# Performance work log

Hardware: AMD Instinct MI355X
Metric: run time of the kernel (lower is better)

Reference implementation:

```python
import jax, jax.numpy as jnp
import numpy as np

N = 10000   # nodes
E = 160000  # edges
F_IN = 768  # input features
EPS = 1e-5


def _norm_weights(src, dst, ew, n):
    # sym-normalized scaled Laplacian with lambda_max=2: T_hat = -D^{-1/2} A D^{-1/2}
    deg = jax.ops.segment_sum(ew, src, num_segments=n)
    deg_safe = jnp.where(deg > 0, deg, 1.0)
    dis = jnp.where(deg > 0, jax.lax.rsqrt(deg_safe), 0.0)
    return -dis[src] * ew * dis[dst]


def _cheb(x, src, dst, norm, Ws, b, n):
    # PyG ChebConv forward: out = sum_k lin_k(T_k(L_hat) x) + bias
    def prop(h):  # gather -> weight -> scatter-add
        return jax.ops.segment_sum(norm[:, None] * h[src], dst, num_segments=n)
    Tx0 = x
    out = Tx0 @ Ws[0]
    if len(Ws) > 1:
        Tx1 = prop(Tx0)
        out = out + Tx1 @ Ws[1]
        for W in Ws[2:]:
            Tx2 = 2.0 * prop(Tx1) - Tx0
            out = out + Tx2 @ W
            Tx0, Tx1 = Tx1, Tx2
    return out + b


def _bn(x, g, b):
    # training-mode batch norm over the node dim
    mu = x.mean(axis=0)
    var = x.var(axis=0)
    return (x - mu) * jax.lax.rsqrt(var + EPS) * g + b


def _glorot(k, shp):
    lim = (6.0 / (shp[0] + shp[1])) ** 0.5
    return jax.random.uniform(k, shp, jnp.float32, -lim, lim)


def setup_inputs() -> dict:
    key = jax.random.key(0)
    ks = jax.random.split(key, 12)
    inp = {
        "x": jax.random.normal(ks[0], (N, F_IN), jnp.float32),
        "edge_index": jax.random.randint(ks[1], (2, E), 0, N, jnp.int64),
        "edge_attr": jax.random.uniform(ks[2], (E,), jnp.float32),
        "W1_0": _glorot(ks[3], (F_IN, 512)), "b1": jnp.zeros((512,), jnp.float32),
        "g1": jnp.ones((512,), jnp.float32), "be1": jnp.zeros((512,), jnp.float32),
        "W2_0": _glorot(ks[4], (512, 256)), "W2_1": _glorot(ks[5], (512, 256)),
        "b2": jnp.zeros((256,), jnp.float32),
        "g2": jnp.ones((256,), jnp.float32), "be2": jnp.zeros((256,), jnp.float32),
        "W3_0": _glorot(ks[6], (256, 128)), "W3_1": _glorot(ks[7], (256, 128)),
        "W3_2": _glorot(ks[8], (256, 128)), "b3": jnp.zeros((128,), jnp.float32),
        "g3": jnp.ones((128,), jnp.float32), "be3": jnp.zeros((128,), jnp.float32),
        "fcW": _glorot(ks[9], (128, 6)), "fcb": jnp.zeros((6,), jnp.float32),
    }
    return inp


def reference(x, edge_index, edge_attr,
              W1_0, b1, g1, be1,
              W2_0, W2_1, b2, g2, be2,
              W3_0, W3_1, W3_2, b3, g3, be3,
              fcW, fcb):
    src, dst = edge_index[0], edge_index[1]
    norm = _norm_weights(src, dst, edge_attr, N)
    h = jax.nn.relu(_bn(_cheb(x, src, dst, norm, [W1_0], b1, N), g1, be1))
    h = jax.nn.relu(_bn(_cheb(h, src, dst, norm, [W2_0, W2_1], b2, N), g2, be2))
    h = _bn(_cheb(h, src, dst, norm, [W3_0, W3_1, W3_2], b3, N), g3, be3)
    return jax.nn.log_softmax(h @ fcW + fcb, axis=1)
```

## Files before the change

### kernel.cpp

```cpp
#include <hip/hip_runtime.h>
#include <hip/hip_bf16.h>
#include <cstdint>

#define N_NODES 10000
#define N_EDGES 160000
#define MPAD    10112

typedef __attribute__((ext_vector_type(8))) short short8;
typedef __attribute__((ext_vector_type(4))) float floatx4;
typedef unsigned short us;


__device__ __forceinline__ us bf16_rn(float f) {
    union { float f; unsigned u; } c{f};
    unsigned r = c.u + 0x7FFF + ((c.u >> 16) & 1);
    return (us)(r >> 16);
}
__device__ __forceinline__ float bf16_to_f(us h) {
    union { unsigned u; float f; } c{(unsigned)h << 16};
    return c.f;
}
__device__ __forceinline__ unsigned pack_hi2(float a, float b) {
    return (unsigned)bf16_rn(a) | ((unsigned)bf16_rn(b) << 16);
}
__device__ __forceinline__ unsigned pack_lo2(float a, float b) {
    float ra = a - bf16_to_f(bf16_rn(a));
    float rb = b - bf16_to_f(bf16_rn(b));
    return (unsigned)bf16_rn(ra) | ((unsigned)bf16_rn(rb) << 16);
}

__device__ __forceinline__ void gload_lds16(const void* g, void* l) {
    __builtin_amdgcn_global_load_lds(
        (const __attribute__((address_space(1))) unsigned int*)g,
        (__attribute__((address_space(3))) unsigned int*)l, 16, 0, 0);
}



__global__ void deg_kernel(const int* __restrict__ src, const int* __restrict__ dst,
                           const float* __restrict__ ew,
                           float* __restrict__ deg, int* __restrict__ cnt) {
    int e = blockIdx.x * blockDim.x + threadIdx.x;
    if (e >= N_EDGES) return;
    atomicAdd(&deg[src[e]], ew[e]);
    atomicAdd(&cnt[dst[e]], 1);
}

__global__ __launch_bounds__(1024) void dis_scan_kernel(const float* __restrict__ deg,
                                                        const int* __restrict__ cnt,
                                                        float* __restrict__ dis,
                                                        int* __restrict__ rowptr) {
    const int t = threadIdx.x;
    if (blockIdx.x != 0) {
        int n = (blockIdx.x - 1) * 1024 + t;
        if (n < N_NODES) {
            float d = deg[n];
            dis[n] = d > 0.f ? rsqrtf(d) : 0.f;
        }
        return;
    }
    __shared__ int wsum[16];
    const int lane = t & 63, wid = t >> 6;
    int carry = 0;
    for (int base = 0; base < N_NODES; base += 1024) {
        int i = base + t;
        int v = (i < N_NODES) ? cnt[i] : 0;
        int s = v;
        #pragma unroll
        for (int off = 1; off < 64; off <<= 1) {
            int u = __shfl_up(s, off);
            if (lane >= off) s += u;
        }
        if (lane == 63) wsum[wid] = s;
        __syncthreads();
        int woff = 0, tot = 0;
        for (int ww = 0; ww < 16; ++ww) {
            int xv = wsum[ww];
            if (ww < wid) woff += xv;
            tot += xv;
        }
        if (i < N_NODES) rowptr[i + 1] = carry + woff + s;
        carry += tot;
        __syncthreads();
    }
    if (t == 0) rowptr[0] = 0;
}

__global__ void fill_kernel(const int* __restrict__ src, const int* __restrict__ dst,
                            const float* __restrict__ ew, const float* __restrict__ dis,
                            const int* __restrict__ rowptr, int* __restrict__ fill,
                            int* __restrict__ csr_src, float* __restrict__ csr_w) {
    int e = blockIdx.x * blockDim.x + threadIdx.x;
    if (e >= N_EDGES) return;
    int s = src[e], d = dst[e];
    int pos = rowptr[d] + atomicAdd(&fill[d], 1);
    csr_src[pos] = s;
    csr_w[pos] = -dis[s] * ew[e] * dis[d];
}


__device__ __forceinline__ void cvt_x_body(int bx, int k16, const float* __restrict__ x,
                                           us* __restrict__ Ap) {
    int m = bx * 256 + threadIdx.x;
    if (m >= N_NODES) return;
    const float4* p = (const float4*)(x + (size_t)m * 768 + k16 * 16);
    float4 v0 = p[0], v1 = p[1], v2 = p[2], v3 = p[3];
    uint4 hi0, hi1, lo0, lo1;
    hi0.x = pack_hi2(v0.x, v0.y); hi0.y = pack_hi2(v0.z, v0.w);
    hi0.z = pack_hi2(v1.x, v1.y); hi0.w = pack_hi2(v1.z, v1.w);
    hi1.x = pack_hi2(v2.x, v2.y); hi1.y = pack_hi2(v2.z, v2.w);
    hi1.z = pack_hi2(v3.x, v3.y); hi1.w = pack_hi2(v3.z, v3.w);
    lo0.x = pack_lo2(v0.x, v0.y); lo0.y = pack_lo2(v0.z, v0.w);
    lo0.z = pack_lo2(v1.x, v1.y); lo0.w = pack_lo2(v1.z, v1.w);
    lo1.x = pack_lo2(v2.x, v2.y); lo1.y = pack_lo2(v2.z, v2.w);
    lo1.z = pack_lo2(v3.x, v3.y); lo1.w = pack_lo2(v3.z, v3.w);
    int pa = m >> 7, rr = m & 127;
    int kt = k16 >> 1, kqb = (k16 & 1) * 2;
    size_t th = ((size_t)pa * 48 + kt) * 4096;
    size_t tl = ((size_t)pa * 48 + 24 + kt) * 4096;
    *(uint4*)&Ap[th + ((kqb + 0) * 128 + rr) * 8] = hi0;
    *(uint4*)&Ap[th + ((kqb + 1) * 128 + rr) * 8] = hi1;
    *(uint4*)&Ap[tl + ((kqb + 0) * 128 + rr) * 8] = lo0;
    *(uint4*)&Ap[tl + ((kqb + 1) * 128 + rr) * 8] = lo1;
}

__device__ __forceinline__ void cvt_w_body(int bx, int k16, const float* __restrict__ W,
                                           us* __restrict__ Bp, int K, int N) {
    int n = bx * 256 + threadIdx.x;
    if (n >= N) return;
    float v[16];
    #pragma unroll
    for (int j = 0; j < 16; ++j) v[j] = W[(size_t)(k16 * 16 + j) * N + n];
    uint4 hi0, hi1, lo0, lo1;
    hi0.x = pack_hi2(v[0], v[1]);  hi0.y = pack_hi2(v[2], v[3]);
    hi0.z = pack_hi2(v[4], v[5]);  hi0.w = pack_hi2(v[6], v[7]);
    hi1.x = pack_hi2(v[8], v[9]);  hi1.y = pack_hi2(v[10], v[11]);
    hi1.z = pack_hi2(v[12], v[13]); hi1.w = pack_hi2(v[14], v[15]);
    lo0.x = pack_lo2(v[0], v[1]);  lo0.y = pack_lo2(v[2], v[3]);
    lo0.z = pack_lo2(v[4], v[5]);  lo0.w = pack_lo2(v[6], v[7]);
    lo1.x = pack_lo2(v[8], v[9]);  lo1.y = pack_lo2(v[10], v[11]);
    lo1.z = pack_lo2(v[12], v[13]); lo1.w = pack_lo2(v[14], v[15]);
    int pb = n >> 6, c = n & 63;
    int NKTB = K >> 4;
    int kt = k16 >> 1, kqb = (k16 & 1) * 2;
    size_t th = ((size_t)pb * NKTB + kt) * 2048;
    size_t tl = ((size_t)pb * NKTB + (K >> 5) + kt) * 2048;
    *(uint4*)&Bp[th + ((kqb + 0) * 64 + c) * 8] = hi0;
    *(uint4*)&Bp[th + ((kqb + 1) * 64 + c) * 8] = hi1;
    *(uint4*)&Bp[tl + ((kqb + 0) * 64 + c) * 8] = lo0;
    *(uint4*)&Bp[tl + ((kqb + 1) * 64 + c) * 8] = lo1;
}

__global__ __launch_bounds__(256) void cvt_all_kernel(const float* __restrict__ x,
                                                      us* __restrict__ A1,
                                                      const float* __restrict__ W1,
                                                      us* __restrict__ B1T,
                                                      const float* __restrict__ W2a,
                                                      const float* __restrict__ W2b,
                                                      us* __restrict__ B2T,
                                                      const float* __restrict__ W3a,
                                                      const float* __restrict__ W3b,
                                                      const float* __restrict__ W3c,
                                                      us* __restrict__ B3T) {
    int b = blockIdx.x;
    if (b < 1920) { cvt_x_body(b % 40, b / 40, x, A1); return; }
    b -= 1920;
    if (b < 96)  { cvt_w_body(b & 1, b >> 1, W1, B1T, 768, 512); return; }
    b -= 96;
    if (b < 32)  { cvt_w_body(0, b, W2a, B2T, 512, 256); return; }
    b -= 32;
    if (b < 32)  { cvt_w_body(0, b, W2b, B2T + (size_t)4 * 32 * 2048, 512, 256); return; }
    b -= 32;
    if (b < 16)  { cvt_w_body(0, b, W3a, B3T, 256, 128); return; }
    b -= 16;
    if (b < 16)  { cvt_w_body(0, b, W3b, B3T + (size_t)2 * 16 * 2048, 256, 128); return; }
    b -= 16;
    cvt_w_body(0, b, W3c, B3T + (size_t)4 * 16 * 2048, 256, 128);
}

__global__ __launch_bounds__(256) void bn_relu_cvt_kernel(const float* __restrict__ G,
                                                          const float* __restrict__ sums,
                                                          const float* __restrict__ g,
                                                          const float* __restrict__ be,
                                                          us* __restrict__ Ap, int F) {
    const int k16 = blockIdx.y;
    int m = blockIdx.x * 256 + threadIdx.x;
    if (m >= N_NODES) return;
    const float invM = 1.0f / (float)N_NODES;
    float sc[16], sh[16];
    #pragma unroll
    for (int j = 0; j < 16; ++j) {
        int c = k16 * 16 + j;
        float mu = sums[c] * invM;
        float s = g[c] * rsqrtf(sums[F + c] * invM - mu * mu + 1e-5f);
        sc[j] = s;
        sh[j] = be[c] - mu * s;
    }
    const float4* p = (const float4*)(G + (size_t)m * F + k16 * 16);
    float v[16];
    #pragma unroll
    for (int q = 0; q < 4; ++q) {
        float4 t4 = p[q];
        v[q * 4 + 0] = t4.x; v[q * 4 + 1] = t4.y;
        v[q * 4 + 2] = t4.z; v[q * 4 + 3] = t4.w;
    }
    #pragma unroll
    for (int j = 0; j < 16; ++j) v[j] = fmaxf(v[j] * sc[j] + sh[j], 0.f);
    uint4 hi0, hi1, lo0, lo1;
    hi0.x = pack_hi2(v[0], v[1]);  hi0.y = pack_hi2(v[2], v[3]);
    hi0.z = pack_hi2(v[4], v[5]);  hi0.w = pack_hi2(v[6], v[7]);
    hi1.x = pack_hi2(v[8], v[9]);  hi1.y = pack_hi2(v[10], v[11]);
    hi1.z = pack_hi2(v[12], v[13]); hi1.w = pack_hi2(v[14], v[15]);
    lo0.x = pack_lo2(v[0], v[1]);  lo0.y = pack_lo2(v[2], v[3]);
    lo0.z = pack_lo2(v[4], v[5]);  lo0.w = pack_lo2(v[6], v[7]);
    lo1.x = pack_lo2(v[8], v[9]);  lo1.y = pack_lo2(v[10], v[11]);
    lo1.z = pack_lo2(v[12], v[13]); lo1.w = pack_lo2(v[14], v[15]);
    int pa = m >> 7, rr = m & 127;
    int NKT = F >> 4;
    int kt = k16 >> 1, kqb = (k16 & 1) * 2;
    size_t th = ((size_t)pa * NKT + kt) * 4096;
    size_t tl = ((size_t)pa * NKT + (F >> 5) + kt) * 4096;
    *(uint4*)&Ap[th + ((kqb + 0) * 128 + rr) * 8] = hi0;
    *(uint4*)&Ap[th + ((kqb + 1) * 128 + rr) * 8] = hi1;
    *(uint4*)&Ap[tl + ((kqb + 0) * 128 + rr) * 8] = lo0;
    *(uint4*)&Ap[tl + ((kqb + 1) * 128 + rr) * 8] = lo1;
}


__global__ __launch_bounds__(256, 4) void mfma_gemm_kernel(
        const us* __restrict__ Ap,
        const us* __restrict__ BpT,
        float* __restrict__ C,
        int M, int Ksub, int Nc, int ncb,
        float* __restrict__ sums) {
    __shared__ us As[4096];
    __shared__ us Bs[2048];
    const int t = threadIdx.x;
    const int w = t >> 6, l = t & 63;

    int nwg = gridDim.x, bid = blockIdx.x;
    int q = nwg >> 3, r = nwg & 7;
    int xcd = bid & 7, idx = bid >> 3;
    int wgid = (xcd < r ? xcd * (q + 1) : r * (q + 1) + (xcd - r) * q) + idx;
    const int row0 = (wgid / ncb) * 128;
    const int col0 = (wgid % ncb) * 64;

    const int NKTA = Ksub >> 4;
    const int Ktot = 3 * Ksub;
    const int wr = w >> 1, wc = w & 1;
    const int lr = l & 15, kq = l >> 4;

    const size_t Abase = (size_t)(row0 >> 7) * NKTA * 4096;
    const size_t Bbase = (size_t)(col0 >> 6) * NKTA * 2048;

    floatx4 acc[4][2] = {};

    for (int k0 = 0; k0 < Ktot; k0 += 32) {
        int kA = (k0 < 2 * Ksub) ? k0 : k0 - 2 * Ksub;
        int kB = (k0 < Ksub)     ? k0 : k0 - Ksub;
        const us* At = Ap + Abase + (size_t)(kA >> 5) * 4096;
        const us* Bt = BpT + Bbase + (size_t)(kB >> 5) * 2048;
        gload_lds16(At + (w * 64 + l) * 8,       (char*)As + w * 1024);
        gload_lds16(At + ((w + 4) * 64 + l) * 8, (char*)As + (w + 4) * 1024);
        gload_lds16(Bt + (w * 64 + l) * 8,       (char*)Bs + w * 1024);
        __syncthreads();
        short8 af[4], bfr[2];
        #pragma unroll
        for (int m = 0; m < 4; ++m)
            af[m] = *(const short8*)&As[(kq * 128 + wr * 64 + m * 16 + lr) * 8];
        #pragma unroll
        for (int n = 0; n < 2; ++n)
            bfr[n] = *(const short8*)&Bs[(kq * 64 + wc * 32 + n * 16 + lr) * 8];
        #pragma unroll
        for (int m = 0; m < 4; ++m)
            #pragma unroll
            for (int n = 0; n < 2; ++n)
                acc[m][n] = __builtin_amdgcn_mfma_f32_16x16x32_bf16(
                    af[m], bfr[n], acc[m][n], 0, 0, 0);
        __syncthreads();
    }

    #pragma unroll
    for (int m = 0; m < 4; ++m) {
        int rb = row0 + wr * 64 + m * 16 + kq * 4;
        #pragma unroll
        for (int j = 0; j < 4; ++j) {
            int rr = rb + j;
            if (rr < M) {
                #pragma unroll
                for (int n = 0; n < 2; ++n)
                    C[(size_t)rr * Nc + col0 + wc * 32 + n * 16 + lr] = acc[m][n][j];
            }
        }
    }

    if (sums) {
        float s[2] = {0.f, 0.f}, qv[2] = {0.f, 0.f};
        #pragma unroll
        for (int m = 0; m < 4; ++m)
            #pragma unroll
            for (int n = 0; n < 2; ++n)
                #pragma unroll
                for (int j = 0; j < 4; ++j) {
                    float v = acc[m][n][j];
                    s[n] += v; qv[n] += v * v;
                }
        float* red = (float*)As;
        int g8 = wr * 4 + kq;
        #pragma unroll
        for (int n = 0; n < 2; ++n) {
            int c = wc * 32 + n * 16 + lr;
            red[g8 * 128 + c * 2 + 0] = s[n];
            red[g8 * 128 + c * 2 + 1] = qv[n];
        }
        __syncthreads();
        if (t < 128) {
            float tot = 0.f;
            #pragma unroll
            for (int g = 0; g < 8; ++g) tot += red[g * 128 + t];
            int c = t >> 1, e = t & 1;
            atomicAdd(&sums[e * 512 + col0 + c], tot);
        }
    }
}


__global__ __launch_bounds__(256) void prop_l2_stats_kernel(const float* __restrict__ G2,
                                                            const int* __restrict__ rowptr,
                                                            const int* __restrict__ csr_s,
                                                            const float* __restrict__ csr_w,
                                                            float* __restrict__ out2,
                                                            float* __restrict__ sums) {
    const int f = threadIdx.x;
    float s = 0.f, qv = 0.f;
    #pragma unroll 1
    for (int nn = 0; nn < 16; ++nn) {
        const int n = blockIdx.x * 16 + nn;
        const int e1 = rowptr[n + 1];
        float acc = 0.f;
        int e = rowptr[n];
        for (; e + 1 < e1; e += 2) {
            int s0 = csr_s[e], s1 = csr_s[e + 1];
            float w0 = csr_w[e], w1 = csr_w[e + 1];
            acc += w0 * G2[(size_t)s0 * 512 + 256 + f] + w1 * G2[(size_t)s1 * 512 + 256 + f];
        }
        if (e < e1) acc += csr_w[e] * G2[(size_t)csr_s[e] * 512 + 256 + f];
        float v = acc + G2[(size_t)n * 512 + f];
        out2[(size_t)n * 256 + f] = v;
        s += v; qv += v * v;
    }
    atomicAdd(&sums[f], s);
    atomicAdd(&sums[256 + f], qv);
}

__global__ __launch_bounds__(256) void prop_f128_kernel(const float* __restrict__ H,
                                                        int ldH, int offH,
                                                        const float* __restrict__ H2,
                                                        float s2,
                                                        const int* __restrict__ rowptr,
                                                        const int* __restrict__ csr_s,
                                                        const float* __restrict__ csr_w,
                                                        float* __restrict__ out) {
    const int n = blockIdx.x * 2 + (threadIdx.x >> 7);
    const int f = threadIdx.x & 127;
    const int e1 = rowptr[n + 1];
    float acc = 0.f;
    if (H2) {
        for (int e = rowptr[n]; e < e1; ++e) {
            int s = csr_s[e];
            acc += csr_w[e] * (H[(size_t)s * ldH + offH + f] + s2 * H2[(size_t)s * 128 + f]);
        }
    } else {
        int e = rowptr[n];
        for (; e + 1 < e1; e += 2) {
            int s0 = csr_s[e], s1 = csr_s[e + 1];
            acc += csr_w[e] * H[(size_t)s0 * ldH + offH + f]
                 + csr_w[e + 1] * H[(size_t)s1 * ldH + offH + f];
        }
        if (e < e1) acc += csr_w[e] * H[(size_t)csr_s[e] * ldH + offH + f];
    }
    out[(size_t)n * 128 + f] = acc;
}

__global__ __launch_bounds__(128) void combine3_stats_kernel(const float* __restrict__ G3,
                                                             const float* __restrict__ U,
                                                             float* __restrict__ Fbuf,
                                                             float* __restrict__ sums) {
    const int t = threadIdx.x;
    int r0 = blockIdx.x * 80, r1 = min(r0 + 80, N_NODES);
    float s = 0.f, q = 0.f;
    for (int r = r0; r < r1; ++r) {
        float v = G3[(size_t)r * 384 + t] - G3[(size_t)r * 384 + 256 + t]
                + U[(size_t)r * 128 + t];
        Fbuf[(size_t)r * 128 + t] = v;
        s += v; q += v * v;
    }
    atomicAdd(&sums[t], s);
    atomicAdd(&sums[128 + t], q);
}


__global__ __launch_bounds__(256) void final_kernel(const float* __restrict__ h,
                                                    const float* __restrict__ sums,
                                                    const float* __restrict__ g3,
                                                    const float* __restrict__ be3,
                                                    const float* __restrict__ fcW,
                                                    const float* __restrict__ fcb,
                                                    float* __restrict__ out) {
    const int t = threadIdx.x, lane = t & 63, wid = t >> 6;
    const int r = blockIdx.x * 4 + wid;
    if (r >= N_NODES) return;
    const float invM = 1.0f / (float)N_NODES;
    float v[6] = {0.f, 0.f, 0.f, 0.f, 0.f, 0.f};
    #pragma unroll
    for (int kk = 0; kk < 2; ++kk) {
        int k = lane + kk * 64;
        float mu = sums[k] * invM;
        float sc = g3[k] * rsqrtf(sums[128 + k] * invM - mu * mu + 1e-5f);
        float sh = be3[k] - mu * sc;
        float x = h[(size_t)r * 128 + k] * sc + sh;
        #pragma unroll
        for (int j = 0; j < 6; ++j) v[j] += x * fcW[k * 6 + j];
    }
    #pragma unroll
    for (int j = 0; j < 6; ++j)
        #pragma unroll
        for (int off = 32; off > 0; off >>= 1) v[j] += __shfl_down(v[j], off);
    if (lane == 0) {
        #pragma unroll
        for (int j = 0; j < 6; ++j) v[j] += fcb[j];
        float m = v[0];
        #pragma unroll
        for (int j = 1; j < 6; ++j) m = fmaxf(m, v[j]);
        float s = 0.f;
        #pragma unroll
        for (int j = 0; j < 6; ++j) s += expf(v[j] - m);
        float l = m + logf(s);
        #pragma unroll
        for (int j = 0; j < 6; ++j) out[r * 6 + j] = v[j] - l;
    }
}


extern "C" void kernel_launch(void* const* d_in, const int* in_sizes, int n_in,
                              void* d_out, int out_size, void* d_ws, size_t ws_size,
                              hipStream_t stream) {
    (void)in_sizes; (void)n_in; (void)out_size; (void)ws_size;
    const float* x   = (const float*)d_in[0];
    const int*   ei  = (const int*)d_in[1];
    const float* ea  = (const float*)d_in[2];
    const float* W1  = (const float*)d_in[3];
    const float* g1  = (const float*)d_in[5];
    const float* be1 = (const float*)d_in[6];
    const float* W2a = (const float*)d_in[7];
    const float* W2b = (const float*)d_in[8];
    const float* g2  = (const float*)d_in[10];
    const float* be2 = (const float*)d_in[11];
    const float* W3a = (const float*)d_in[12];
    const float* W3b = (const float*)d_in[13];
    const float* W3c = (const float*)d_in[14];
    const float* g3  = (const float*)d_in[16];
    const float* be3 = (const float*)d_in[17];
    const float* fcW = (const float*)d_in[18];
    const float* fcb = (const float*)d_in[19];
    float* out = (float*)d_out;

    const int* src = ei;
    const int* dst = ei + N_EDGES;

    char* w = (char*)d_ws;
    size_t off = 0;
    auto alloc = [&](size_t bytes) -> void* {
        void* p = w + off;
        off += (bytes + 4095) & ~(size_t)4095;
        return p;
    };
    float* deg    = (float*)alloc(N_NODES * 4);
    int*   cnt    = (int*)  alloc(N_NODES * 4);
    int*   fillc  = (int*)  alloc(N_NODES * 4);
    float* sums1  = (float*)alloc(1024 * 4);
    float* sums2  = (float*)alloc(1024 * 4);
    float* sums3  = (float*)alloc(1024 * 4);
    size_t zero_bytes = off;
    float* dis    = (float*)alloc(N_NODES * 4);
    int*   rowptr = (int*)  alloc((N_NODES + 1) * 4);
    int*   csr_s  = (int*)  alloc(N_EDGES * 4);
    float* csr_w  = (float*)alloc(N_EDGES * 4);
    us* B1T = (us*)alloc((size_t)512 * 1536 * 2);
    us* B2T = (us*)alloc((size_t)512 * 1024 * 2);
    us* B3T = (us*)alloc((size_t)384 * 512 * 2);
    us* slotA = (us*)alloc((size_t)MPAD * 1536 * 2);
    float* slotG = (float*)alloc((size_t)N_NODES * 512 * 4);
    float* slotC = (float*)alloc((size_t)N_NODES * 256 * 4);
    float* bufF  = (float*)alloc((size_t)N_NODES * 128 * 4);

    us* A1 = slotA;
    us* A2 = slotA;
    us* A3 = slotA;
    float* G1 = slotG;
    float* G2 = slotG;
    float* G3 = slotG;
    float* out2 = slotC;
    float* bufT = slotC;
    float* bufU = slotC + (size_t)N_NODES * 128;

    hipMemsetAsync(d_ws, 0, zero_bytes, stream);

    deg_kernel<<<N_EDGES / 256, 256, 0, stream>>>(src, dst, ea, deg, cnt);
    dis_scan_kernel<<<40, 1024, 0, stream>>>(deg, cnt, dis, rowptr);
    fill_kernel<<<N_EDGES / 256, 256, 0, stream>>>(src, dst, ea, dis, rowptr, fillc,
                                                   csr_s, csr_w);

    cvt_all_kernel<<<2128, 256, 0, stream>>>(x, A1, W1, B1T, W2a, W2b, B2T,
                                             W3a, W3b, W3c, B3T);

    mfma_gemm_kernel<<<632, 256, 0, stream>>>(A1, B1T, G1, N_NODES, 768, 512, 8, sums1);
    bn_relu_cvt_kernel<<<dim3(40, 32), 256, 0, stream>>>(G1, sums1, g1, be1, A2, 512);

    mfma_gemm_kernel<<<632, 256, 0, stream>>>(A2, B2T, G2, N_NODES, 512, 512, 8, nullptr);
    prop_l2_stats_kernel<<<625, 256, 0, stream>>>(G2, rowptr, csr_s, csr_w, out2, sums2);
    bn_relu_cvt_kernel<<<dim3(40, 16), 256, 0, stream>>>(out2, sums2, g2, be2, A3, 256);

    mfma_gemm_kernel<<<474, 256, 0, stream>>>(A3, B3T, G3, N_NODES, 256, 384, 6, nullptr);
    prop_f128_kernel<<<N_NODES / 2, 256, 0, stream>>>(G3, 384, 256, nullptr, 0.f,
                                                      rowptr, csr_s, csr_w, bufT);
    prop_f128_kernel<<<N_NODES / 2, 256, 0, stream>>>(G3, 384, 128, bufT, 2.f,
                                                      rowptr, csr_s, csr_w, bufU);
    combine3_stats_kernel<<<125, 128, 0, stream>>>(G3, bufU, bufF, sums3);

    final_kernel<<<2500, 256, 0, stream>>>(bufF, sums3, g3, be3, fcW, fcb, out);
}
```

Before: 429.7 us.

## Vectorize SpMM propagation with float4 per-node warps and fuse layer-3 combine

Rewrites the graph propagation kernels so each node is handled by a sub-group of 64 or 32 lanes that load float4 feature slices. This gives more parallelism and wider memory accesses than the old one-thread-per-feature scheme, where layer 2 processed 16 nodes serially per block. Layer-2 batch-norm statistics move to a separate reduction kernel. The second layer-3 propagation now also does the combine and the per-block statistics reduction, which removes the combine kernel and the intermediate U buffer. In exchange there is one extra pass over out2 for statistics, and more atomics in layer 3.

```diff
diff --git a/kernel.cpp b/kernel.cpp
--- a/kernel.cpp
+++ b/kernel.cpp
@@ -325,78 +325,117 @@
 }
 
 
-__global__ __launch_bounds__(256) void prop_l2_stats_kernel(const float* __restrict__ G2,
-                                                            const int* __restrict__ rowptr,
-                                                            const int* __restrict__ csr_s,
-                                                            const float* __restrict__ csr_w,
-                                                            float* __restrict__ out2,
-                                                            float* __restrict__ sums) {
-    const int f = threadIdx.x;
-    float s = 0.f, qv = 0.f;
-    #pragma unroll 1
-    for (int nn = 0; nn < 16; ++nn) {
-        const int n = blockIdx.x * 16 + nn;
-        const int e1 = rowptr[n + 1];
-        float acc = 0.f;
-        int e = rowptr[n];
-        for (; e + 1 < e1; e += 2) {
-            int s0 = csr_s[e], s1 = csr_s[e + 1];
-            float w0 = csr_w[e], w1 = csr_w[e + 1];
-            acc += w0 * G2[(size_t)s0 * 512 + 256 + f] + w1 * G2[(size_t)s1 * 512 + 256 + f];
-        }
-        if (e < e1) acc += csr_w[e] * G2[(size_t)csr_s[e] * 512 + 256 + f];
-        float v = acc + G2[(size_t)n * 512 + f];
-        out2[(size_t)n * 256 + f] = v;
-        s += v; qv += v * v;
-    }
-    atomicAdd(&sums[f], s);
-    atomicAdd(&sums[256 + f], qv);
-}
-
-__global__ __launch_bounds__(256) void prop_f128_kernel(const float* __restrict__ H,
-                                                        int ldH, int offH,
-                                                        const float* __restrict__ H2,
-                                                        float s2,
-                                                        const int* __restrict__ rowptr,
-                                                        const int* __restrict__ csr_s,
-                                                        const float* __restrict__ csr_w,
-                                                        float* __restrict__ out) {
-    const int n = blockIdx.x * 2 + (threadIdx.x >> 7);
-    const int f = threadIdx.x & 127;
+__global__ __launch_bounds__(256) void prop_l2_kernel(const float* __restrict__ G2,
+                                                      const int* __restrict__ rowptr,
+                                                      const int* __restrict__ csr_s,
+                                                      const float* __restrict__ csr_w,
+                                                      float* __restrict__ out2) {
+    const int g = threadIdx.x >> 6, lane = threadIdx.x & 63;
+    const int n = blockIdx.x * 4 + g;
+    const int f4 = lane * 4;
+    float4 acc = {0.f, 0.f, 0.f, 0.f};
+    int e = rowptr[n];
     const int e1 = rowptr[n + 1];
-    float acc = 0.f;
-    if (H2) {
-        for (int e = rowptr[n]; e < e1; ++e) {
-            int s = csr_s[e];
-            acc += csr_w[e] * (H[(size_t)s * ldH + offH + f] + s2 * H2[(size_t)s * 128 + f]);
-        }
-    } else {
-        int e = rowptr[n];
-        for (; e + 1 < e1; e += 2) {
-            int s0 = csr_s[e], s1 = csr_s[e + 1];
-            acc += csr_w[e] * H[(size_t)s0 * ldH + offH + f]
-                 + csr_w[e + 1] * H[(size_t)s1 * ldH + offH + f];
-        }
-        if (e < e1) acc += csr_w[e] * H[(size_t)csr_s[e] * ldH + offH + f];
-    }
-    out[(size_t)n * 128 + f] = acc;
-}
-
-__global__ __launch_bounds__(128) void combine3_stats_kernel(const float* __restrict__ G3,
-                                                             const float* __restrict__ U,
+    for (; e + 1 < e1; e += 2) {
+        int s0 = csr_s[e], s1 = csr_s[e + 1];
+        float w0 = csr_w[e], w1 = csr_w[e + 1];
+        float4 a = *(const float4*)&G2[(size_t)s0 * 512 + 256 + f4];
+        float4 b = *(const float4*)&G2[(size_t)s1 * 512 + 256 + f4];
+        acc.x += w0 * a.x + w1 * b.x; acc.y += w0 * a.y + w1 * b.y;
+        acc.z += w0 * a.z + w1 * b.z; acc.w += w0 * a.w + w1 * b.w;
+    }
+    if (e < e1) {
+        float w0 = csr_w[e];
+        float4 a = *(const float4*)&G2[(size_t)csr_s[e] * 512 + 256 + f4];
+        acc.x += w0 * a.x; acc.y += w0 * a.y; acc.z += w0 * a.z; acc.w += w0 * a.w;
+    }
+    float4 base = *(const float4*)&G2[(size_t)n * 512 + f4];
+    acc.x += base.x; acc.y += base.y; acc.z += base.z; acc.w += base.w;
+    *(float4*)&out2[(size_t)n * 256 + f4] = acc;
+}
+
+__global__ __launch_bounds__(256) void bn_stats256_kernel(const float* __restrict__ h,
+                                                          float* __restrict__ sums) {
+    const int t = threadIdx.x;
+    int r0 = blockIdx.x * 20, r1 = min(r0 + 20, N_NODES);
+    float s = 0.f, q = 0.f;
+    for (int r = r0; r < r1; ++r) {
+        float v = h[(size_t)r * 256 + t];
+        s += v; q += v * v;
+    }
+    atomicAdd(&sums[t], s);
+    atomicAdd(&sums[256 + t], q);
+}
+
+__global__ __launch_bounds__(256) void prop3a_kernel(const float* __restrict__ G3,
+                                                     const int* __restrict__ rowptr,
+                                                     const int* __restrict__ csr_s,
+                                                     const float* __restrict__ csr_w,
+                                                     float* __restrict__ T) {
+    const int g = threadIdx.x >> 5, lane = threadIdx.x & 31;
+    const int n = blockIdx.x * 8 + g;
+    const int f4 = lane * 4;
+    float4 acc = {0.f, 0.f, 0.f, 0.f};
+    int e = rowptr[n];
+    const int e1 = rowptr[n + 1];
+    for (; e + 1 < e1; e += 2) {
+        int s0 = csr_s[e], s1 = csr_s[e + 1];
+        float w0 = csr_w[e], w1 = csr_w[e + 1];
+        float4 a = *(const float4*)&G3[(size_t)s0 * 384 + 256 + f4];
+        float4 b = *(const float4*)&G3[(size_t)s1 * 384 + 256 + f4];
+        acc.x += w0 * a.x + w1 * b.x; acc.y += w0 * a.y + w1 * b.y;
+        acc.z += w0 * a.z + w1 * b.z; acc.w += w0 * a.w + w1 * b.w;
+    }
+    if (e < e1) {
+        float w0 = csr_w[e];
+        float4 a = *(const float4*)&G3[(size_t)csr_s[e] * 384 + 256 + f4];
+        acc.x += w0 * a.x; acc.y += w0 * a.y; acc.z += w0 * a.z; acc.w += w0 * a.w;
+    }
+    *(float4*)&T[(size_t)n * 128 + f4] = acc;
+}
+
+__global__ __launch_bounds__(256) void prop3b_combine_kernel(const float* __restrict__ G3,
+                                                             const float* __restrict__ T,
+                                                             const int* __restrict__ rowptr,
+                                                             const int* __restrict__ csr_s,
+                                                             const float* __restrict__ csr_w,
                                                              float* __restrict__ Fbuf,
                                                              float* __restrict__ sums) {
+    __shared__ float red_s[8][128];
+    __shared__ float red_q[8][128];
+    const int g = threadIdx.x >> 5, lane = threadIdx.x & 31;
+    const int n = blockIdx.x * 8 + g;
+    const int f4 = lane * 4;
+    float4 acc = {0.f, 0.f, 0.f, 0.f};
+    int e = rowptr[n];
+    const int e1 = rowptr[n + 1];
+    for (; e < e1; ++e) {
+        int s = csr_s[e];
+        float w0 = csr_w[e];
+        float4 a = *(const float4*)&G3[(size_t)s * 384 + 128 + f4];
+        float4 b = *(const float4*)&T[(size_t)s * 128 + f4];
+        acc.x += w0 * (a.x + 2.f * b.x); acc.y += w0 * (a.y + 2.f * b.y);
+        acc.z += w0 * (a.z + 2.f * b.z); acc.w += w0 * (a.w + 2.f * b.w);
+    }
+    float4 p = *(const float4*)&G3[(size_t)n * 384 + f4];
+    float4 r = *(const float4*)&G3[(size_t)n * 384 + 256 + f4];
+    float4 v;
+    v.x = p.x - r.x + acc.x; v.y = p.y - r.y + acc.y;
+    v.z = p.z - r.z + acc.z; v.w = p.w - r.w + acc.w;
+    *(float4*)&Fbuf[(size_t)n * 128 + f4] = v;
+    red_s[g][f4 + 0] = v.x; red_s[g][f4 + 1] = v.y;
+    red_s[g][f4 + 2] = v.z; red_s[g][f4 + 3] = v.w;
+    red_q[g][f4 + 0] = v.x * v.x; red_q[g][f4 + 1] = v.y * v.y;
+    red_q[g][f4 + 2] = v.z * v.z; red_q[g][f4 + 3] = v.w * v.w;
+    __syncthreads();
     const int t = threadIdx.x;
-    int r0 = blockIdx.x * 80, r1 = min(r0 + 80, N_NODES);
-    float s = 0.f, q = 0.f;
-    for (int r = r0; r < r1; ++r) {
-        float v = G3[(size_t)r * 384 + t] - G3[(size_t)r * 384 + 256 + t]
-                + U[(size_t)r * 128 + t];
-        Fbuf[(size_t)r * 128 + t] = v;
-        s += v; q += v * v;
-    }
-    atomicAdd(&sums[t], s);
-    atomicAdd(&sums[128 + t], q);
+    if (t < 128) {
+        float s = 0.f, q = 0.f;
+        #pragma unroll
+        for (int gg = 0; gg < 8; ++gg) { s += red_s[gg][t]; q += red_q[gg][t]; }
+        atomicAdd(&sums[t], s);
+        atomicAdd(&sums[128 + t], q);
+    }
 }
 
 
@@ -502,7 +541,6 @@
     float* G3 = slotG;
     float* out2 = slotC;
     float* bufT = slotC;
-    float* bufU = slotC + (size_t)N_NODES * 128;
 
     hipMemsetAsync(d_ws, 0, zero_bytes, stream);
 
@@ -518,15 +556,14 @@
     bn_relu_cvt_kernel<<<dim3(40, 32), 256, 0, stream>>>(G1, sums1, g1, be1, A2, 512);
 
     mfma_gemm_kernel<<<632, 256, 0, stream>>>(A2, B2T, G2, N_NODES, 512, 512, 8, nullptr);
-    prop_l2_stats_kernel<<<625, 256, 0, stream>>>(G2, rowptr, csr_s, csr_w, out2, sums2);
+    prop_l2_kernel<<<2500, 256, 0, stream>>>(G2, rowptr, csr_s, csr_w, out2);
+    bn_stats256_kernel<<<500, 256, 0, stream>>>(out2, sums2);
     bn_relu_cvt_kernel<<<dim3(40, 16), 256, 0, stream>>>(out2, sums2, g2, be2, A3, 256);
 
     mfma_gemm_kernel<<<474, 256, 0, stream>>>(A3, B3T, G3, N_NODES, 256, 384, 6, nullptr);
-    prop_f128_kernel<<<N_NODES / 2, 256, 0, stream>>>(G3, 384, 256, nullptr, 0.f,
-                                                      rowptr, csr_s, csr_w, bufT);
-    prop_f128_kernel<<<N_NODES / 2, 256, 0, stream>>>(G3, 384, 128, bufT, 2.f,
-                                                      rowptr, csr_s, csr_w, bufU);
-    combine3_stats_kernel<<<125, 128, 0, stream>>>(G3, bufU, bufF, sums3);
+    prop3a_kernel<<<1250, 256, 0, stream>>>(G3, rowptr, csr_s, csr_w, bufT);
+    prop3b_combine_kernel<<<1250, 256, 0, stream>>>(G3, bufT, rowptr, csr_s, csr_w,
+                                                    bufF, sums3);
 
     final_kernel<<<2500, 256, 0, stream>>>(bufF, sums3, g3, be3, fcW, fcb, out);
 }
```

Measured after the change: 385.3 us. -10.3%, faster.
